# Performance work log

Hardware: AMD Instinct MI355X
Metric: run time of the kernel (lower is better)

The kernel has to match this reference:

```python
import jax, jax.numpy as jnp
import numpy as np

EPS = 1.1920929e-07  # torch clamp_probs eps for float32
TEMP = 0.3           # sampler temperature T


def conv1d(x, w, b, pad):
    # x: [B, Cin, L], w: [Cout, Cin, K] -> [B, Cout, L']
    y = jax.lax.conv_general_dilated(x, w, window_strides=(1,), padding=[(pad, pad)],
                                     dimension_numbers=('NCH', 'OIH', 'NCH'))
    return y + b[None, :, None]


def setup_inputs() -> dict:
    key = jax.random.key(0)
    ks = jax.random.split(key, 20)
    B, L, V, E, F, H, K = 512, 512, 100000, 100, 100, 100, 10
    p = lambda i, shape: jax.random.normal(ks[i], shape, jnp.float32) * 0.02
    return {
        'x': jax.random.randint(ks[0], (B, L), 0, V, dtype=jnp.int32),
        'u': jax.random.uniform(ks[1], (B, K, L), dtype=jnp.float32),
        'emb': p(2, (V, E)),
        'conv1_w': p(3, (F, E, 3)), 'conv1_b': p(4, (F,)),
        'gi_w': p(5, (H, F)), 'gi_b': p(6, (H,)),
        'conv2_w': p(7, (H, F, 3)), 'conv2_b': p(8, (H,)),
        'li_w': p(9, (H, H, 3)), 'li_b': p(10, (H,)),
        'conv3_w': p(11, (F, 2 * H, 1)), 'conv3_b': p(12, (F,)),
        'conv4_w': p(13, (1, F, 1)), 'conv4_b': p(14, (1,)),
        'fc1_w': p(15, (H, E)), 'fc1_b': p(16, (H,)),
        'head_w': p(17, (1, H)), 'head_b': p(18, (1,)),
    }


def _ti_logits(e, conv1_w, conv1_b, gi_w, gi_b, conv2_w, conv2_b,
               li_w, li_b, conv3_w, conv3_b, conv4_w, conv4_b):
    relu = jax.nn.relu
    xt = jnp.swapaxes(e, 1, 2)                       # [B, E, L]
    h = relu(conv1d(xt, conv1_w, conv1_b, 1))        # [B, F, L]
    g = relu(h.mean(axis=-1) @ gi_w.T + gi_b)        # [B, H] (AdaptiveAvgPool1d(1))
    loc = relu(conv1d(relu(conv1d(h, conv2_w, conv2_b, 1)), li_w, li_b, 1))  # [B, H, L]
    gexp = jnp.broadcast_to(g[:, :, None], loc.shape)
    z = jnp.concatenate([gexp, loc], axis=1)         # [B, 2H, L]
    z = relu(conv1d(z, conv3_w, conv3_b, 0))
    return conv1d(z, conv4_w, conv4_b, 0)            # [B, 1, L]


def reference(x, u, emb, conv1_w, conv1_b, gi_w, gi_b, conv2_w, conv2_b,
              li_w, li_b, conv3_w, conv3_b, conv4_w, conv4_b,
              fc1_w, fc1_b, head_w, head_b):
    e = emb[x]                                       # [B, L, E] embedding gather
    logits = _ti_logits(e, conv1_w, conv1_b, gi_w, gi_b, conv2_w, conv2_b,
                        li_w, li_b, conv3_w, conv3_b, conv4_w, conv4_b)
    # Gumbel top-k continuous sampling (training path)
    uc = jnp.clip(u, EPS, 1.0 - EPS)
    gumbel = -jnp.log(-jnp.log(uc))                  # [B, K, L]
    noisy = (gumbel + logits) / TEMP                 # logits [B,1,L] broadcasts over K
    csamples = jax.nn.softmax(noisy, axis=-1).max(axis=1)  # [B, L]
    # distil predictor: masked mean pooling + MLP + sigmoid head
    pooled = (e * csamples[:, :, None]).mean(axis=1)  # [B, E]
    h = jax.nn.relu(pooled @ fc1_w.T + fc1_b)
    out = jax.nn.sigmoid(h @ head_w.T + head_b)       # [B, 1]
    return out, csamples
```

## Files before the change

### kernel.cpp

```cpp
#include <hip/hip_runtime.h>
#include <math.h>

#define DEV __device__ __forceinline__

typedef __attribute__((ext_vector_type(8))) short short8;
typedef __attribute__((ext_vector_type(4))) short short4v;
typedef __attribute__((ext_vector_type(4))) float f32x4;
typedef __attribute__((ext_vector_type(2))) unsigned uint2v;

#define SSTR 136
#define ROWB (16 * SSTR * 2)

DEV short f2bf(float f) {
    unsigned u = __builtin_bit_cast(unsigned, f);
    unsigned r = (u + 0x7fffu + ((u >> 16) & 1u)) >> 16;
    return (short)r;
}

#if __has_builtin(__builtin_amdgcn_cvt_pk_bf16_f32)
DEV unsigned pk2bf(float a, float b) {
    auto v = __builtin_amdgcn_cvt_pk_bf16_f32(a, b);
    return __builtin_bit_cast(unsigned, v);
}
#else
DEV unsigned pk2bf(float a, float b) {
    return ((unsigned)(unsigned short)f2bf(a)) |
           (((unsigned)(unsigned short)f2bf(b)) << 16);
}
#endif

DEV float bfu(short s) {
    unsigned u = ((unsigned)(unsigned short)s) << 16;
    return __builtin_bit_cast(float, u);
}

__global__ __launch_bounds__(256) void prep_kernel(
    const float* __restrict__ emb, short* __restrict__ embT,
    const float* __restrict__ c1w, const float* __restrict__ c2w,
    const float* __restrict__ liw, const float* __restrict__ c3w,
    const float* __restrict__ giw,
    short* __restrict__ A1, short* __restrict__ A2,
    short* __restrict__ A3, short* __restrict__ A4,
    float* __restrict__ giwT, float* __restrict__ w3T) {
    int bxg = blockIdx.x;
    if (bxg < 12500) {
        int t = threadIdx.x;
        int row = bxg * 8 + (t >> 5);
        int c4 = t & 31;
        if (c4 >= 28) return;
        short4v v = {0, 0, 0, 0};
        if (c4 < 25) {
            f32x4 e = *(const f32x4*)&emb[row * 100 + c4 * 4];
#pragma unroll
            for (int r = 0; r < 4; ++r) v[r] = f2bf(e[r]);
        }
        *(short4v*)&embT[row * 112 + c4 * 4] = v;
        return;
    }
    if (bxg >= 12738) {
        int t = threadIdx.x;
        if (bxg == 12738) {
            for (int i = t; i < 10000; i += 256) {
                int f = i / 100, g = i % 100;
                giwT[f * 100 + g] = giw[g * 100 + f];
            }
        } else {
            for (int i = t; i < 10000; i += 256) {
                int h = i / 100, f = i % 100;
                w3T[h * 100 + f] = c3w[f * 200 + h];
            }
        }
        return;
    }
    if (threadIdx.x >= 64) return;
    int bx = bxg - 12500;
    const float* w; short* dst; int mode, lbx;
    if (bx < 70)       { w = c1w; dst = A1; mode = 0; lbx = bx; }
    else if (bx < 140) { w = c2w; dst = A2; mode = 0; lbx = bx - 70; }
    else if (bx < 210) { w = liw; dst = A3; mode = 0; lbx = bx - 140; }
    else               { w = c3w; dst = A4; mode = 1; lbx = bx - 210; }
    int lane = threadIdx.x;
    int f = lbx % 7 * 16 + (lane & 15);
    int kb = (lbx / 7) * 32 + (lane >> 4) * 8;
    short8 v;
#pragma unroll
    for (int j = 0; j < 8; ++j) {
        int kk = kb + j;
        float val = 0.f;
        if (f < 100) {
            if (mode == 0) {
                int oct = kk >> 3, dk = oct / 13;
                int c = (oct - 13 * dk) * 8 + (kk & 7);
                if (dk < 3 && c < 100) val = w[(f * 100 + c) * 3 + dk];
            } else {
                if (kk < 100) val = w[f * 200 + 100 + kk];
            }
        }
        v[j] = f2bf(val);
    }
    *(short8*)&dst[(lbx * 64 + lane) * 8] = v;
}

template<int MT, int NT, int MTB, int NTB, bool CLAMPL, bool POOL,
         bool TO_GLOBAL, bool EDGE>
DEV void ctap(const short* __restrict__ Ap, const short* s_src, short* s_dst,
              short* __restrict__ gout, const int* bofs, const int* bofs4,
              const float* __restrict__ bias, int row0l, int l0,
              float* __restrict__ hpart_slot, int lane) {
    const int q = lane >> 4, n = lane & 15;
    const f32x4 z4 = {0.f, 0.f, 0.f, 0.f};
    f32x4 acc[MT][NT];
#pragma unroll
    for (int mt = 0; mt < MT; ++mt) {
        int fb = (MTB + mt) * 16 + q * 4;
        f32x4 bs = (fb < 100) ? *(const f32x4*)&bias[fb] : z4;
#pragma unroll
        for (int nt = 0; nt < NT; ++nt) acc[mt][nt] = bs;
    }
#pragma unroll
    for (int ks = 0; ks < 10; ++ks) {
        short8 a[MT];
#pragma unroll
        for (int mt = 0; mt < MT; ++mt)
            a[mt] = *(const short8*)&Ap[(ks * 448 + (MTB + mt) * 64 + lane) * 8];
        const char* bp = (const char*)s_src + bofs[ks];
        short8 bf[NT];
#pragma unroll
        for (int nt = 0; nt < NT; ++nt) {
            if (CLAMPL && (NTB + nt) == 4)
                bf[nt] = *(const short8*)((const char*)s_src + bofs4[ks]);
            else
                bf[nt] = *(const short8*)(bp + (NTB + nt) * ROWB);
        }
#pragma unroll
        for (int mt = 0; mt < MT; ++mt)
#pragma unroll
            for (int nt = 0; nt < NT; ++nt)
                acc[mt][nt] = __builtin_amdgcn_mfma_f32_16x16x32_bf16(
                    a[mt], bf[nt], acc[mt][nt], 0, 0, 0);
    }
    f32x4 ps[MT];
    if constexpr (POOL) {
#pragma unroll
        for (int mt = 0; mt < MT; ++mt) ps[mt] = z4;
    }
#pragma unroll
    for (int nt = 0; nt < NT; ++nt) {
        const int j = (NTB + nt) * 16 + n;
        const int l = row0l + j;
        bool lok = true;
        if constexpr (EDGE) lok = ((unsigned)l < 512u);
        const bool pok = POOL && (l >= l0) && (l < l0 + 64);
#pragma unroll
        for (int mt = 0; mt < MT; ++mt) {
            const int fb = (MTB + mt) * 16 + q * 4;
            f32x4 v;
#pragma unroll
            for (int r = 0; r < 4; ++r) {
                v[r] = fmaxf(acc[mt][nt][r], 0.f);
                if constexpr (EDGE) v[r] = lok ? v[r] : 0.f;
            }
            if constexpr (POOL) {
                if (pok) {
#pragma unroll
                    for (int r = 0; r < 4; ++r) ps[mt][r] += v[r];
                }
            }
            uint2v pk;
            pk[0] = pk2bf(v[0], v[1]); pk[1] = pk2bf(v[2], v[3]);
            if constexpr (TO_GLOBAL) {
                *(uint2v*)&gout[j * 112 + fb] = pk;
            } else {
                if ((NTB + nt) < 4 || n < 6)
                    *(uint2v*)&s_dst[j * SSTR + fb] = pk;
            }
        }
    }
    if constexpr (POOL) {
#pragma unroll
        for (int mt = 0; mt < MT; ++mt)
#pragma unroll
            for (int off = 1; off <= 8; off <<= 1)
#pragma unroll
                for (int r = 0; r < 4; ++r)
                    ps[mt][r] += __shfl_xor(ps[mt][r], off, 64);
        if (n == 0) {
#pragma unroll
            for (int mt = 0; mt < MT; ++mt)
                *(f32x4*)&hpart_slot[(MTB + mt) * 16 + q * 4] = ps[mt];
        }
    }
}

__global__ __launch_bounds__(256, 4) void fused_conv_kernel(
    const int* __restrict__ xidx, const short* __restrict__ embT,
    const short* __restrict__ A1, const short* __restrict__ A2,
    const short* __restrict__ A3,
    const float* __restrict__ b1, const float* __restrict__ b2,
    const float* __restrict__ b3,
    short* __restrict__ locT, float* __restrict__ hpart) {
    extern __shared__ char smem[];
    short* s_e = (short*)smem;
    short* s_h = (short*)(smem + 72 * SSTR * 2);
    const int tid = threadIdx.x;
    const int b = blockIdx.y, bx = blockIdx.x, l0 = bx * 64;
    const int lane = tid & 63, wv = tid >> 6;
    const int q = lane >> 4, n = lane & 15;

#pragma unroll
    for (int p = 0; p < 5; ++p) {
        int idx = tid + p * 256;
        int j = idx >> 4, c8 = idx & 15;
        if (j < 70 && c8 < 14) {
            int lg = l0 - 3 + j;
            short8 v = {0, 0, 0, 0, 0, 0, 0, 0};
            if (lg >= 0 && lg < 512) {
                int row = xidx[b * 512 + lg];
                v = *(const short8*)&embT[row * 112 + c8 * 8];
            }
            *(short8*)&s_e[j * SSTR + c8 * 8] = v;
        }
    }

    int bofs[10], bofs4[10];
#pragma unroll
    for (int ks = 0; ks < 10; ++ks) {
        int oct = ks * 4 + q;
        int dk = (oct >= 39) ? 3 : (oct >= 26) ? 2 : (oct >= 13) ? 1 : 0;
        int c0 = (oct - 13 * dk) * 8;
        bofs[ks] = ((n + dk) * SSTR + c0) * 2;
        int r4 = 64 + n + dk; if (r4 > 69) r4 = 69;
        bofs4[ks] = (r4 * SSTR + c0) * 2;
    }
    float* hps = hpart + ((b * 8 + bx) * 2 + (wv & 1)) * 112;
    short* gouts = locT + ((size_t)b * 512 + l0) * 112;

    __syncthreads();
    const bool edge = (bx == 0) || (bx == 7);

#define PASS3T(Ap, SRC, DST, BIAS, R0L, PL, E)                                   \
    if (wv == 0)      ctap<4,3,0,0,false,PL,false,E>(Ap,SRC,DST,nullptr,bofs,bofs4,BIAS,R0L,l0,hps,lane); \
    else if (wv == 1) ctap<4,2,0,3,true, PL,false,E>(Ap,SRC,DST,nullptr,bofs,bofs4,BIAS,R0L,l0,hps,lane); \
    else if (wv == 2) ctap<3,3,4,0,false,PL,false,E>(Ap,SRC,DST,nullptr,bofs,bofs4,BIAS,R0L,l0,hps,lane); \
    else              ctap<3,2,4,3,true, PL,false,E>(Ap,SRC,DST,nullptr,bofs,bofs4,BIAS,R0L,l0,hps,lane);

    if (edge) {
        PASS3T(A1, s_e, s_h, b1, l0 - 2, true, true)
        __syncthreads();
        PASS3T(A2, s_h, s_e, b2, l0 - 1, false, true)
    } else {
        PASS3T(A1, s_e, s_h, b1, l0 - 2, true, false)
        __syncthreads();
        PASS3T(A2, s_h, s_e, b2, l0 - 1, false, false)
    }
    __syncthreads();
    if (wv == 0)      ctap<4,2,0,0,false,false,true,false>(A3,s_e,nullptr,gouts,bofs,bofs4,b3,l0,l0,hps,lane);
    else if (wv == 1) ctap<4,2,0,2,false,false,true,false>(A3,s_e,nullptr,gouts,bofs,bofs4,b3,l0,l0,hps,lane);
    else if (wv == 2) ctap<3,2,4,0,false,false,true,false>(A3,s_e,nullptr,gouts,bofs,bofs4,b3,l0,l0,hps,lane);
    else              ctap<3,2,4,2,false,false,true,false>(A3,s_e,nullptr,gouts,bofs,bofs4,b3,l0,l0,hps,lane);
#undef PASS3T
}

template<int NTB>
DEV void c3tile(const short* __restrict__ locB, float* s_part,
                const short* __restrict__ A4, const float* s_zg,
                const float* __restrict__ w4, int lane) {
    const int q = lane >> 4, n = lane & 15;
    const f32x4 z4 = {0.f, 0.f, 0.f, 0.f};
    f32x4 acc[7][2];
#pragma unroll
    for (int mt = 0; mt < 7; ++mt) {
        int fb = mt * 16 + q * 4;
        f32x4 zgv = *(const f32x4*)&s_zg[fb];
#pragma unroll
        for (int nt = 0; nt < 2; ++nt) acc[mt][nt] = zgv;
    }
#pragma unroll
    for (int ks = 0; ks < 4; ++ks) {
        short8 a[7];
#pragma unroll
        for (int mt = 0; mt < 7; ++mt)
            a[mt] = *(const short8*)&A4[(ks * 448 + mt * 64 + lane) * 8];
        int c0 = (ks * 4 + q) * 8;
        if (c0 > 104) c0 = 104;
        const short* bp = locB + n * 112 + c0;
        short8 bf[2];
#pragma unroll
        for (int nt = 0; nt < 2; ++nt)
            bf[nt] = *(const short8*)(bp + (NTB + nt) * 16 * 112);
#pragma unroll
        for (int mt = 0; mt < 7; ++mt)
#pragma unroll
            for (int nt = 0; nt < 2; ++nt)
                acc[mt][nt] = __builtin_amdgcn_mfma_f32_16x16x32_bf16(
                    a[mt], bf[nt], acc[mt][nt], 0, 0, 0);
    }
#pragma unroll
    for (int nt = 0; nt < 2; ++nt) {
        float part = 0.f;
#pragma unroll
        for (int mt = 0; mt < 7; ++mt) {
            const int fb = mt * 16 + q * 4;
            f32x4 w4v = (fb < 100) ? *(const f32x4*)&w4[fb] : z4;
#pragma unroll
            for (int r = 0; r < 4; ++r)
                part += fmaxf(acc[mt][nt][r], 0.f) * w4v[r];
        }
        part += __shfl_xor(part, 16, 64);
        part += __shfl_xor(part, 32, 64);
        if (q == 0) s_part[(NTB + nt) * 16 + n] = part;
    }
}

__global__ __launch_bounds__(256, 4) void conv3_logits_kernel(
    const short* __restrict__ locT, const short* __restrict__ A4,
    const float* __restrict__ hpart, const float* __restrict__ giwT,
    const float* __restrict__ gi_b, const float* __restrict__ w3T,
    const float* __restrict__ b3, const float* __restrict__ w4,
    const float* __restrict__ b4, float* __restrict__ logits) {
    __shared__ float s_part[128];
    __shared__ float s_zg[112];
    __shared__ float s_hm[112];
    __shared__ float s_g[100];
    const int tid = threadIdx.x;
    const int b = blockIdx.y, l0r = blockIdx.x * 128;
    const int lane = tid & 63, wv = tid >> 6;

    if (tid < 112) {
        float a = 0.f;
#pragma unroll
        for (int s = 0; s < 16; ++s) a += hpart[(b * 16 + s) * 112 + tid];
        s_hm[tid] = a * (1.f / 512.f);
    }
    __syncthreads();
    if (tid < 100) {
        float a = gi_b[tid];
        for (int f = 0; f < 100; ++f) a += s_hm[f] * giwT[f * 100 + tid];
        s_g[tid] = fmaxf(a, 0.f);
    }
    __syncthreads();
    if (tid < 112) {
        float a = 0.f;
        if (tid < 100) {
            a = b3[tid];
            for (int h = 0; h < 100; ++h) a += s_g[h] * w3T[h * 100 + tid];
        }
        s_zg[tid] = a;
    }
    __syncthreads();

    const short* locB = locT + ((size_t)b * 512 + l0r) * 112;
    if (wv == 0)      c3tile<0>(locB, s_part, A4, s_zg, w4, lane);
    else if (wv == 1) c3tile<2>(locB, s_part, A4, s_zg, w4, lane);
    else if (wv == 2) c3tile<4>(locB, s_part, A4, s_zg, w4, lane);
    else              c3tile<6>(locB, s_part, A4, s_zg, w4, lane);
    __syncthreads();
    if (tid < 128)
        logits[b * 512 + l0r + tid] = s_part[tid] + b4[0];
}

__global__ __launch_bounds__(512) void samp_head_kernel(
    const float* __restrict__ u, const float* __restrict__ logits,
    const int* __restrict__ xidx, const short* __restrict__ embT,
    const float* __restrict__ f1w, const float* __restrict__ f1b,
    const float* __restrict__ hw, const float* __restrict__ hb,
    float* __restrict__ cs_out, float* __restrict__ out) {
    const float EPSV = 1.1920929e-07f;
    const float INVT = 1.f / 0.3f;
    int b = blockIdx.x, tid = threadIdx.x;
    int lane = tid & 63, wv = tid >> 6;
    __shared__ float s_logT[512], s_cs[512];
    __shared__ int s_x[512];
    __shared__ float s_csw[8][512];
    __shared__ float s_acc[32][112];
    __shared__ float s_pool[112], s_h2[100], s_fin[8];
    if (tid < 512) {
        s_logT[tid] = logits[b * 512 + tid] * INVT;
        s_x[tid] = xidx[b * 512 + tid];
    }
    __syncthreads();
    const int nk = (wv < 2) ? 2 : 1;
    float csl[8];
#pragma unroll
    for (int i = 0; i < 8; ++i) csl[i] = 0.f;
    float lt[8];
#pragma unroll
    for (int i = 0; i < 8; ++i) lt[i] = s_logT[lane * 8 + i];
    for (int j = 0; j < nk; ++j) {
        int k = wv + 8 * j;
        f32x4 u0 = *(const f32x4*)&u[(b * 10 + k) * 512 + lane * 8];
        f32x4 u1 = *(const f32x4*)&u[(b * 10 + k) * 512 + lane * 8 + 4];
        float nz[8];
#pragma unroll
        for (int i = 0; i < 8; ++i) {
            float vv = (i < 4) ? u0[i] : u1[i - 4];
            vv = fminf(fmaxf(vv, EPSV), 1.f - EPSV);
            nz[i] = -__logf(-__logf(vv)) * INVT + lt[i];
        }
        float m = nz[0];
#pragma unroll
        for (int i = 1; i < 8; ++i) m = fmaxf(m, nz[i]);
#pragma unroll
        for (int off = 1; off <= 32; off <<= 1) m = fmaxf(m, __shfl_xor(m, off, 64));
        float e[8], s = 0.f;
#pragma unroll
        for (int i = 0; i < 8; ++i) { e[i] = __expf(nz[i] - m); s += e[i]; }
#pragma unroll
        for (int off = 1; off <= 32; off <<= 1) s += __shfl_xor(s, off, 64);
        float inv = 1.f / s;
#pragma unroll
        for (int i = 0; i < 8; ++i) csl[i] = fmaxf(csl[i], e[i] * inv);
    }
#pragma unroll
    for (int i = 0; i < 8; ++i) s_csw[wv][lane * 8 + i] = csl[i];
    __syncthreads();
    if (tid < 512) {
        float c = s_csw[0][tid];
#pragma unroll
        for (int w = 1; w < 8; ++w) c = fmaxf(c, s_csw[w][tid]);
        s_cs[tid] = c;
        cs_out[b * 512 + tid] = c;
    }
    __syncthreads();
    int jg = tid >> 4, c8 = tid & 15;
    if (c8 < 14) {
        f32x4 pa = {0.f, 0.f, 0.f, 0.f}, pb = {0.f, 0.f, 0.f, 0.f};
#pragma unroll 4
        for (int l = jg; l < 512; l += 32) {
            int row = s_x[l];
            float cv = s_cs[l];
            short8 e8 = *(const short8*)&embT[(size_t)row * 112 + c8 * 8];
#pragma unroll
            for (int r = 0; r < 4; ++r) {
                pa[r] += cv * bfu(e8[r]);
                pb[r] += cv * bfu(e8[4 + r]);
            }
        }
        *(f32x4*)&s_acc[jg][c8 * 8] = pa;
        *(f32x4*)&s_acc[jg][c8 * 8 + 4] = pb;
    }
    __syncthreads();
    if (tid < 112) {
        float p = 0.f;
#pragma unroll
        for (int g = 0; g < 32; ++g) p += s_acc[g][tid];
        s_pool[tid] = p * (1.f / 512.f);
    }
    __syncthreads();
    if (tid < 100) {
        float a = f1b[tid];
        for (int i = 0; i < 100; ++i) a += s_pool[i] * f1w[tid * 100 + i];
        s_h2[tid] = fmaxf(a, 0.f);
    }
    __syncthreads();
    float v = (tid < 100) ? s_h2[tid] * hw[tid] : 0.f;
#pragma unroll
    for (int off = 32; off >= 1; off >>= 1) v += __shfl_xor(v, off, 64);
    if (lane == 0) s_fin[wv] = v;
    __syncthreads();
    if (tid == 0) {
        float z = hb[0];
#pragma unroll
        for (int w = 0; w < 8; ++w) z += s_fin[w];
        out[b] = 1.f / (1.f + __expf(-z));
    }
}

extern "C" void kernel_launch(void* const* d_in, const int* in_sizes, int n_in,
                              void* d_out, int out_size, void* d_ws, size_t ws_size,
                              hipStream_t stream) {
    const int*   x   = (const int*)d_in[0];
    const float* u   = (const float*)d_in[1];
    const float* emb = (const float*)d_in[2];
    const float* c1w = (const float*)d_in[3];
    const float* c1b = (const float*)d_in[4];
    const float* giw = (const float*)d_in[5];
    const float* gib = (const float*)d_in[6];
    const float* c2w = (const float*)d_in[7];
    const float* c2b = (const float*)d_in[8];
    const float* liw = (const float*)d_in[9];
    const float* lib = (const float*)d_in[10];
    const float* c3w = (const float*)d_in[11];
    const float* c3b = (const float*)d_in[12];
    const float* c4w = (const float*)d_in[13];
    const float* c4b = (const float*)d_in[14];
    const float* f1w = (const float*)d_in[15];
    const float* f1b = (const float*)d_in[16];
    const float* hww = (const float*)d_in[17];
    const float* hbb = (const float*)d_in[18];
    float* out = (float*)d_out;

    char* ws = (char*)d_ws;
    short* locT   = (short*)(ws + 0);
    short* embT   = (short*)(ws + 58720256);
    short* A1     = (short*)(ws + 81120256);
    short* A2     = (short*)(ws + 81191936);
    short* A3     = (short*)(ws + 81263616);
    short* A4     = (short*)(ws + 81335296);
    float* logits = (float*)(ws + 81593344);
    float* hpart  = (float*)(ws + 82641920);
    float* giwT   = (float*)(ws + 86311936);
    float* w3T    = (float*)(ws + 86351936);

    prep_kernel<<<12740, 256, 0, stream>>>(emb, embT, c1w, c2w, liw, c3w, giw,
                                           A1, A2, A3, A4, giwT, w3T);

    size_t smemA = (size_t)2 * 72 * SSTR * 2;
    fused_conv_kernel<<<dim3(8, 512), 256, smemA, stream>>>(
        x, embT, A1, A2, A3, c1b, c2b, lib, locT, hpart);
    conv3_logits_kernel<<<dim3(4, 512), 256, 0, stream>>>(
        locT, A4, hpart, giwT, gib, w3T, c3b, c4w, c4b, logits);
    samp_head_kernel<<<512, 512, 0, stream>>>(
        u, logits, x, embT, f1w, f1b, hww, hbb, out + 512, out);
}
```

Measured before the change: 263.8 us.

## Drop bf16 embedding table prep and fuse conv3 logits into sampler kernel

Removes the pass that converted the entire 100000x100 embedding table to a padded bf16 copy. The conv kernel now gathers fp32 rows directly and converts only the looked-up rows in registers, and the pooling stage reads fp32 embeddings. The conv3/logits kernel is merged into the sampling/head kernel, so each 512-thread block computes its batch's logits in shared memory and the logits round-trip through global memory and one launch go away. The trade-off is fewer blocks for the conv3 work, unaligned 13-chunk gathers, and double-width fp32 reads in the gathers.

```diff
diff --git a/kernel.cpp b/kernel.cpp
--- a/kernel.cpp
+++ b/kernel.cpp
@@ -7,6 +7,7 @@
 typedef __attribute__((ext_vector_type(4))) short short4v;
 typedef __attribute__((ext_vector_type(4))) float f32x4;
 typedef __attribute__((ext_vector_type(2))) unsigned uint2v;
+typedef __attribute__((ext_vector_type(4))) unsigned uint4v;
 
 #define SSTR 136
 #define ROWB (16 * SSTR * 2)
@@ -29,13 +30,7 @@
 }
 #endif
 
-DEV float bfu(short s) {
-    unsigned u = ((unsigned)(unsigned short)s) << 16;
-    return __builtin_bit_cast(float, u);
-}
-
 __global__ __launch_bounds__(256) void prep_kernel(
-    const float* __restrict__ emb, short* __restrict__ embT,
     const float* __restrict__ c1w, const float* __restrict__ c2w,
     const float* __restrict__ liw, const float* __restrict__ c3w,
     const float* __restrict__ giw,
@@ -43,23 +38,9 @@
     short* __restrict__ A3, short* __restrict__ A4,
     float* __restrict__ giwT, float* __restrict__ w3T) {
     int bxg = blockIdx.x;
-    if (bxg < 12500) {
+    if (bxg >= 238) {
         int t = threadIdx.x;
-        int row = bxg * 8 + (t >> 5);
-        int c4 = t & 31;
-        if (c4 >= 28) return;
-        short4v v = {0, 0, 0, 0};
-        if (c4 < 25) {
-            f32x4 e = *(const f32x4*)&emb[row * 100 + c4 * 4];
-#pragma unroll
-            for (int r = 0; r < 4; ++r) v[r] = f2bf(e[r]);
-        }
-        *(short4v*)&embT[row * 112 + c4 * 4] = v;
-        return;
-    }
-    if (bxg >= 12738) {
-        int t = threadIdx.x;
-        if (bxg == 12738) {
+        if (bxg == 238) {
             for (int i = t; i < 10000; i += 256) {
                 int f = i / 100, g = i % 100;
                 giwT[f * 100 + g] = giw[g * 100 + f];
@@ -73,7 +54,7 @@
         return;
     }
     if (threadIdx.x >= 64) return;
-    int bx = bxg - 12500;
+    int bx = bxg;
     const float* w; short* dst; int mode, lbx;
     if (bx < 70)       { w = c1w; dst = A1; mode = 0; lbx = bx; }
     else if (bx < 140) { w = c2w; dst = A2; mode = 0; lbx = bx - 70; }
@@ -193,7 +174,7 @@
 }
 
 __global__ __launch_bounds__(256, 4) void fused_conv_kernel(
-    const int* __restrict__ xidx, const short* __restrict__ embT,
+    const int* __restrict__ xidx, const float* __restrict__ emb,
     const short* __restrict__ A1, const short* __restrict__ A2,
     const short* __restrict__ A3,
     const float* __restrict__ b1, const float* __restrict__ b2,
@@ -208,17 +189,25 @@
     const int q = lane >> 4, n = lane & 15;
 
 #pragma unroll
-    for (int p = 0; p < 5; ++p) {
+    for (int p = 0; p < 4; ++p) {
         int idx = tid + p * 256;
-        int j = idx >> 4, c8 = idx & 15;
-        if (j < 70 && c8 < 14) {
+        int j = idx / 13, c8 = idx - j * 13;
+        if (j < 70) {
             int lg = l0 - 3 + j;
-            short8 v = {0, 0, 0, 0, 0, 0, 0, 0};
+            uint4v pk = {0, 0, 0, 0};
             if (lg >= 0 && lg < 512) {
                 int row = xidx[b * 512 + lg];
-                v = *(const short8*)&embT[row * 112 + c8 * 8];
-            }
-            *(short8*)&s_e[j * SSTR + c8 * 8] = v;
+                const float* er = &emb[(size_t)row * 100 + c8 * 8];
+                f32x4 e0 = *(const f32x4*)er;
+                pk[0] = pk2bf(e0[0], e0[1]);
+                pk[1] = pk2bf(e0[2], e0[3]);
+                if (c8 < 12) {
+                    f32x4 e1 = *(const f32x4*)(er + 4);
+                    pk[2] = pk2bf(e1[0], e1[1]);
+                    pk[3] = pk2bf(e1[2], e1[3]);
+                }
+            }
+            *(uint4v*)&s_e[j * SSTR + c8 * 8] = pk;
         }
     }
 
@@ -261,10 +250,9 @@
 #undef PASS3T
 }
 
-template<int NTB>
-DEV void c3tile(const short* __restrict__ locB, float* s_part,
-                const short* __restrict__ A4, const float* s_zg,
-                const float* __restrict__ w4, int lane) {
+DEV void c3t(const short* __restrict__ locB, float* s_part,
+             const short* __restrict__ A4, const float* s_zg,
+             const float* __restrict__ w4, int NTB, int lane) {
     const int q = lane >> 4, n = lane & 15;
     const f32x4 z4 = {0.f, 0.f, 0.f, 0.f};
     f32x4 acc[7][2];
@@ -312,56 +300,14 @@
     }
 }
 
-__global__ __launch_bounds__(256, 4) void conv3_logits_kernel(
+__global__ __launch_bounds__(512) void conv3_samp_kernel(
     const short* __restrict__ locT, const short* __restrict__ A4,
     const float* __restrict__ hpart, const float* __restrict__ giwT,
     const float* __restrict__ gi_b, const float* __restrict__ w3T,
     const float* __restrict__ b3, const float* __restrict__ w4,
-    const float* __restrict__ b4, float* __restrict__ logits) {
-    __shared__ float s_part[128];
-    __shared__ float s_zg[112];
-    __shared__ float s_hm[112];
-    __shared__ float s_g[100];
-    const int tid = threadIdx.x;
-    const int b = blockIdx.y, l0r = blockIdx.x * 128;
-    const int lane = tid & 63, wv = tid >> 6;
-
-    if (tid < 112) {
-        float a = 0.f;
-#pragma unroll
-        for (int s = 0; s < 16; ++s) a += hpart[(b * 16 + s) * 112 + tid];
-        s_hm[tid] = a * (1.f / 512.f);
-    }
-    __syncthreads();
-    if (tid < 100) {
-        float a = gi_b[tid];
-        for (int f = 0; f < 100; ++f) a += s_hm[f] * giwT[f * 100 + tid];
-        s_g[tid] = fmaxf(a, 0.f);
-    }
-    __syncthreads();
-    if (tid < 112) {
-        float a = 0.f;
-        if (tid < 100) {
-            a = b3[tid];
-            for (int h = 0; h < 100; ++h) a += s_g[h] * w3T[h * 100 + tid];
-        }
-        s_zg[tid] = a;
-    }
-    __syncthreads();
-
-    const short* locB = locT + ((size_t)b * 512 + l0r) * 112;
-    if (wv == 0)      c3tile<0>(locB, s_part, A4, s_zg, w4, lane);
-    else if (wv == 1) c3tile<2>(locB, s_part, A4, s_zg, w4, lane);
-    else if (wv == 2) c3tile<4>(locB, s_part, A4, s_zg, w4, lane);
-    else              c3tile<6>(locB, s_part, A4, s_zg, w4, lane);
-    __syncthreads();
-    if (tid < 128)
-        logits[b * 512 + l0r + tid] = s_part[tid] + b4[0];
-}
-
-__global__ __launch_bounds__(512) void samp_head_kernel(
-    const float* __restrict__ u, const float* __restrict__ logits,
-    const int* __restrict__ xidx, const short* __restrict__ embT,
+    const float* __restrict__ b4,
+    const float* __restrict__ u, const int* __restrict__ xidx,
+    const float* __restrict__ emb,
     const float* __restrict__ f1w, const float* __restrict__ f1b,
     const float* __restrict__ hw, const float* __restrict__ hb,
     float* __restrict__ cs_out, float* __restrict__ out) {
@@ -369,16 +315,53 @@
     const float INVT = 1.f / 0.3f;
     int b = blockIdx.x, tid = threadIdx.x;
     int lane = tid & 63, wv = tid >> 6;
+    __shared__ float s_part[512];
+    __shared__ float s_zg[112], s_hm[112], s_g[100];
     __shared__ float s_logT[512], s_cs[512];
     __shared__ int s_x[512];
     __shared__ float s_csw[8][512];
     __shared__ float s_acc[32][112];
     __shared__ float s_pool[112], s_h2[100], s_fin[8];
-    if (tid < 512) {
-        s_logT[tid] = logits[b * 512 + tid] * INVT;
-        s_x[tid] = xidx[b * 512 + tid];
-    }
-    __syncthreads();
+
+    s_x[tid] = xidx[b * 512 + tid];
+
+    if (tid < 112) {
+        float a = 0.f;
+#pragma unroll
+        for (int s = 0; s < 16; ++s) a += hpart[(b * 16 + s) * 112 + tid];
+        s_hm[tid] = a * (1.f / 512.f);
+    }
+    __syncthreads();
+    if (tid < 100) {
+        float a = gi_b[tid];
+        for (int f = 0; f < 100; ++f) a += s_hm[f] * giwT[f * 100 + tid];
+        s_g[tid] = fmaxf(a, 0.f);
+    }
+    __syncthreads();
+    if (tid < 112) {
+        float a = 0.f;
+        if (tid < 100) {
+            a = b3[tid];
+            for (int h = 0; h < 100; ++h) a += s_g[h] * w3T[h * 100 + tid];
+        }
+        s_zg[tid] = a;
+    }
+    __syncthreads();
+
+    {
+        const int t0 = wv >> 2;
+        const int NTB = (wv & 3) * 2;
+#pragma unroll
+        for (int rr = 0; rr < 2; ++rr) {
+            int t = rr * 2 + t0;
+            const short* locB = locT + ((size_t)b * 512 + t * 128) * 112;
+            c3t(locB, s_part + t * 128, A4, s_zg, w4, NTB, lane);
+        }
+    }
+    __syncthreads();
+    s_logT[tid] = (s_part[tid] + b4[0]) * INVT;
+    __syncthreads();
+
     const int nk = (wv < 2) ? 2 : 1;
     float csl[8];
 #pragma unroll
@@ -414,7 +397,7 @@
 #pragma unroll
     for (int i = 0; i < 8; ++i) s_csw[wv][lane * 8 + i] = csl[i];
     __syncthreads();
-    if (tid < 512) {
+    {
         float c = s_csw[0][tid];
 #pragma unroll
         for (int w = 1; w < 8; ++w) c = fmaxf(c, s_csw[w][tid]);
@@ -423,24 +406,27 @@
     }
     __syncthreads();
     int jg = tid >> 4, c8 = tid & 15;
-    if (c8 < 14) {
+    if (c8 < 13) {
         f32x4 pa = {0.f, 0.f, 0.f, 0.f}, pb = {0.f, 0.f, 0.f, 0.f};
 #pragma unroll 4
         for (int l = jg; l < 512; l += 32) {
             int row = s_x[l];
             float cv = s_cs[l];
-            short8 e8 = *(const short8*)&embT[(size_t)row * 112 + c8 * 8];
-#pragma unroll
-            for (int r = 0; r < 4; ++r) {
-                pa[r] += cv * bfu(e8[r]);
-                pb[r] += cv * bfu(e8[4 + r]);
+            const float* er = &emb[(size_t)row * 100 + c8 * 8];
+            f32x4 e0 = *(const f32x4*)er;
+#pragma unroll
+            for (int r = 0; r < 4; ++r) pa[r] += cv * e0[r];
+            if (c8 < 12) {
+                f32x4 e1 = *(const f32x4*)(er + 4);
+#pragma unroll
+                for (int r = 0; r < 4; ++r) pb[r] += cv * e1[r];
             }
         }
         *(f32x4*)&s_acc[jg][c8 * 8] = pa;
         *(f32x4*)&s_acc[jg][c8 * 8 + 4] = pb;
     }
     __syncthreads();
-    if (tid < 112) {
+    if (tid < 100) {
         float p = 0.f;
 #pragma unroll
         for (int g = 0; g < 32; ++g) p += s_acc[g][tid];
@@ -492,24 +478,21 @@
 
     char* ws = (char*)d_ws;
     short* locT   = (short*)(ws + 0);
-    short* embT   = (short*)(ws + 58720256);
-    short* A1     = (short*)(ws + 81120256);
-    short* A2     = (short*)(ws + 81191936);
-    short* A3     = (short*)(ws + 81263616);
-    short* A4     = (short*)(ws + 81335296);
-    float* logits = (float*)(ws + 81593344);
-    float* hpart  = (float*)(ws + 82641920);
-    float* giwT   = (float*)(ws + 86311936);
-    float* w3T    = (float*)(ws + 86351936);
-
-    prep_kernel<<<12740, 256, 0, stream>>>(emb, embT, c1w, c2w, liw, c3w, giw,
-                                           A1, A2, A3, A4, giwT, w3T);
+    short* A1     = (short*)(ws + 58720256);
+    short* A2     = (short*)(ws + 58791936);
+    short* A3     = (short*)(ws + 58863616);
+    short* A4     = (short*)(ws + 58935296);
+    float* hpart  = (float*)(ws + 58963968);
+    float* giwT   = (float*)(ws + 62633984);
+    float* w3T    = (float*)(ws + 62673984);
+
+    prep_kernel<<<240, 256, 0, stream>>>(c1w, c2w, liw, c3w, giw,
+                                         A1, A2, A3, A4, giwT, w3T);
 
     size_t smemA = (size_t)2 * 72 * SSTR * 2;
     fused_conv_kernel<<<dim3(8, 512), 256, smemA, stream>>>(
-        x, embT, A1, A2, A3, c1b, c2b, lib, locT, hpart);
-    conv3_logits_kernel<<<dim3(4, 512), 256, 0, stream>>>(
-        locT, A4, hpart, giwT, gib, w3T, c3b, c4w, c4b, logits);
-    samp_head_kernel<<<512, 512, 0, stream>>>(
-        u, logits, x, embT, f1w, f1b, hww, hbb, out + 512, out);
-}
+        x, emb, A1, A2, A3, c1b, c2b, lib, locT, hpart);
+    conv3_samp_kernel<<<512, 512, 0, stream>>>(
+        locT, A4, hpart, giwT, gib, w3T, c3b, c4w, c4b,
+        u, x, emb, f1w, f1b, hww, hbb, out + 512, out);
+}
```

Result: slower. 273.2 us (+3.6%).
